# Optimization experiments

Hardware: AMD Instinct MI355X
Metric: run time of the kernel (lower is better)

The kernel has to match this reference:

```python
import jax, jax.numpy as jnp
import numpy as np
import math

CEN_W = 1.0
ANG_W = 1.0


def _radius(ndim):
    # Iterative version of the recursive Radius() from the source.
    if ndim < 1:
        raise ValueError('ndim >= 1 required')
    if ndim == 1:
        return 0.0
    r = 0.5
    for _ in range(3, ndim + 1):
        r = 0.5 / math.sqrt(1.0 - r * r)
    return r


def _costheta(ndim):
    return 2.0 * _radius(ndim - 1) ** 2 - 1.0


def setup_inputs() -> dict:
    key = jax.random.key(0)
    k1, k2, k3 = jax.random.split(key, 3)
    B, C, D = 65536, 1000, 512
    y = jax.random.randint(k1, (B,), 0, C, dtype=jnp.int64 if jax.config.jax_enable_x64 else jnp.int32)
    feat = jax.random.normal(k2, (B, D), dtype=jnp.float32)
    centers = jax.random.normal(k3, (C, D), dtype=jnp.float32)
    return {"y": y, "feat": feat, "centers": centers}


def reference(y, feat, centers):
    C = centers.shape[0]
    B = feat.shape[0]
    ct = jnp.float32(_costheta(C))  # static Python constant from num_classes

    # ---- center loss: gather assigned centers, squared diff sum ----
    centers_pred = centers[y]                      # [B, D] gather
    diff = feat - centers_pred
    loss_cen = 0.5 * jnp.sum(diff * diff) / B

    # ---- angular loss: vectorized Gram matrix over classes ----
    # In torch, centers[j].data and dist are detached -> stop_gradient here.
    centers_sg = jax.lax.stop_gradient(centers)
    dist = jnp.linalg.norm(centers_sg, axis=1)     # [C], detached
    gram = centers @ centers_sg.T                  # [C, C]; grad flows via rows only
    sim = gram / (dist[:, None] * dist[None, :])
    offdiag = 1.0 - jnp.eye(C, dtype=sim.dtype)
    loss_ang = jnp.sum(offdiag * (sim - ct) ** 2) / (0.5 * C * (C - 1))

    return loss_cen * CEN_W + loss_ang * ANG_W
```

## Files before the change

### kernel.cpp

```cpp
#include <hip/hip_runtime.h>
#include <math.h>

typedef __attribute__((ext_vector_type(8))) short bf16x8;
typedef __attribute__((ext_vector_type(4))) float f32x4;

__device__ __forceinline__ float wave_reduce(float v) {
#pragma unroll
    for (int off = 32; off > 0; off >>= 1) v += __shfl_down(v, off, 64);
    return v;
}

__device__ __forceinline__ unsigned short f2bf(float x) {
    unsigned u = __float_as_uint(x);
    u += 0x7FFFu + ((u >> 16) & 1u);
    return (unsigned short)(u >> 16);
}

__global__ __launch_bounds__(128) void prep_kernel(const float4* __restrict__ cent4,
                                                   ushort4* __restrict__ xb,
                                                   float* __restrict__ dist2,
                                                   int C, int d4) {
    const int r = blockIdx.x;
    const int t = threadIdx.x;
    __shared__ float sm[2];
    float s = 0.f;
    for (int c = t; c < d4; c += blockDim.x) {
        float4 f = make_float4(0.f, 0.f, 0.f, 0.f);
        if (r < C) f = cent4[(size_t)r * d4 + c];
        s += f.x * f.x + f.y * f.y + f.z * f.z + f.w * f.w;
        ushort4 h;
        h.x = f2bf(f.x); h.y = f2bf(f.y); h.z = f2bf(f.z); h.w = f2bf(f.w);
        xb[(size_t)r * d4 + c] = h;
    }
    s = wave_reduce(s);
    const int lane = t & 63, w = t >> 6;
    if (lane == 0) sm[w] = s;
    __syncthreads();
    if (t == 0) {
        float tot = sm[0];
        if (blockDim.x > 64) tot += sm[1];
        dist2[r] = (r < C) ? tot : 1.0f;
    }
}

__global__ __launch_bounds__(256) void center_kernel(const int* __restrict__ y,
                                                     const float4* __restrict__ feat4,
                                                     const float4* __restrict__ cent4,
                                                     float* __restrict__ out,
                                                     int n4, int d4, float scale) {
    __shared__ float sm[4];
    const int stride = gridDim.x * 256;
    float s = 0.f;
    int i = blockIdx.x * 256 + threadIdx.x;
    if ((stride % d4) == 0) {
        if (i < n4) {
            int row = i / d4;
            const int col = i - row * d4;
            const int rstep = stride / d4;
            for (; i < n4; i += stride, row += rstep) {
                const int cls = y[row];
                float4 f = feat4[i];
                float4 c = cent4[(size_t)cls * d4 + col];
                float dx = f.x - c.x, dy = f.y - c.y, dz = f.z - c.z, dw = f.w - c.w;
                s += dx * dx + dy * dy + dz * dz + dw * dw;
            }
        }
    } else {
        for (; i < n4; i += stride) {
            int row = i / d4;
            int col = i - row * d4;
            const int cls = y[row];
            float4 f = feat4[i];
            float4 c = cent4[(size_t)cls * d4 + col];
            float dx = f.x - c.x, dy = f.y - c.y, dz = f.z - c.z, dw = f.w - c.w;
            s += dx * dx + dy * dy + dz * dz + dw * dw;
        }
    }
    s = wave_reduce(s);
    const int lane = threadIdx.x & 63, w = threadIdx.x >> 6;
    if (lane == 0) sm[w] = s;
    __syncthreads();
    if (threadIdx.x == 0) {
        float tot = sm[0] + sm[1] + sm[2] + sm[3];
        atomicAdd(out, tot * scale);
    }
}

__global__ __launch_bounds__(256) void ang_kernel(const unsigned short* __restrict__ xb,
                                                  const float* __restrict__ dist2,
                                                  float* __restrict__ out,
                                                  int C, int D, int ntile,
                                                  float ct, float scale) {
    __shared__ float sm[4];
    const int wid = threadIdx.x >> 6;
    const int w = blockIdx.x * 4 + wid;
    float local = 0.f;
    if (w < ntile * ntile) {
        const int ti = w / ntile;
        const int tj = w - ti * ntile;
        const int lane = threadIdx.x & 63;
        const int n = lane & 15;
        const int quad = lane >> 4;
        const int dv = D >> 3;
        const bf16x8* ap = (const bf16x8*)xb + (size_t)(ti * 16 + n) * dv + quad;
        const bf16x8* bp = (const bf16x8*)xb + (size_t)(tj * 16 + n) * dv + quad;
        f32x4 acc = {0.f, 0.f, 0.f, 0.f};
        const int steps = D >> 5;
#pragma unroll 8
        for (int st = 0; st < steps; ++st) {
            bf16x8 a = ap[st * 4];
            bf16x8 b = bp[st * 4];
            acc = __builtin_amdgcn_mfma_f32_16x16x32_bf16(a, b, acc, 0, 0, 0);
        }
        const int gj = tj * 16 + n;
        const float dj = dist2[gj];
#pragma unroll
        for (int rr = 0; rr < 4; ++rr) {
            const int gi = ti * 16 + quad * 4 + rr;
            if (gi < C && gj < C && gi != gj) {
                float sim = acc[rr] * rsqrtf(dist2[gi] * dj);
                float dlt = sim - ct;
                local += dlt * dlt;
            }
        }
    }
    local = wave_reduce(local);
    if ((threadIdx.x & 63) == 0) sm[wid] = local;
    __syncthreads();
    if (threadIdx.x == 0) {
        float tot = sm[0] + sm[1] + sm[2] + sm[3];
        atomicAdd(out, tot * scale);
    }
}

extern "C" void kernel_launch(void* const* d_in, const int* in_sizes, int n_in,
                              void* d_out, int out_size, void* d_ws, size_t ws_size,
                              hipStream_t stream) {
    const int* y = (const int*)d_in[0];
    const float* feat = (const float*)d_in[1];
    const float* centers = (const float*)d_in[2];

    const int B = in_sizes[0];
    const int D = in_sizes[1] / B;
    const int C = in_sizes[2] / D;
    const int d4 = D / 4;
    const int ntile = (C + 15) / 16;
    const int Cpad = ntile * 16;

    const int nd = C - 1;
    double r = 0.0;
    if (nd >= 2) {
        r = 0.5;
        for (int i = 3; i <= nd; ++i) r = 0.5 / sqrt(1.0 - r * r);
    }
    const float ct = (float)(2.0 * r * r - 1.0);

    float* outp = (float*)d_out;
    char* ws = (char*)d_ws;
    unsigned short* xb = (unsigned short*)ws;
    size_t xb_bytes = (size_t)Cpad * D * sizeof(unsigned short);
    float* dist2 = (float*)(ws + ((xb_bytes + 255) & ~(size_t)255));

    hipMemsetAsync(d_out, 0, sizeof(float), stream);

    prep_kernel<<<Cpad, 128, 0, stream>>>((const float4*)centers, (ushort4*)xb, dist2, C, d4);

    const int n4 = B * d4;
    const float cen_scale = (float)(0.5 / (double)B);
    center_kernel<<<2048, 256, 0, stream>>>(y, (const float4*)feat, (const float4*)centers,
                                            outp, n4, d4, cen_scale);

    const int ntile2 = ntile * ntile;
    const int ang_blocks = (ntile2 + 3) / 4;
    const float ang_scale = (float)(1.0 / (0.5 * (double)C * (double)(C - 1)));
    ang_kernel<<<ang_blocks, 256, 0, stream>>>(xb, dist2, outp, C, D, ntile, ct, ang_scale);
}
```

Measured before the change: 244.5 us.

## Fuse center and angular kernels into one launch, fold memset into prep

Combines the center-loss and angular-loss kernels into a single launch, with the block index choosing which branch runs, so the compute-heavy MFMA tiles can overlap the bandwidth-bound gather-and-reduce. The hipMemset of the output is dropped; prep_kernel zeroes it instead, which saves one launch. Feature loads become nontemporal to avoid polluting the cache that the centers gather relies on. The extra branching costs little, and the output stays correctly ordered because prep_kernel still runs before the fused kernel on the same stream.

```diff
diff --git a/kernel.cpp b/kernel.cpp
--- a/kernel.cpp
+++ b/kernel.cpp
@@ -3,6 +3,7 @@
 
 typedef __attribute__((ext_vector_type(8))) short bf16x8;
 typedef __attribute__((ext_vector_type(4))) float f32x4;
+typedef __attribute__((ext_vector_type(4))) float vf4;
 
 __device__ __forceinline__ float wave_reduce(float v) {
 #pragma unroll
@@ -19,9 +20,11 @@
 __global__ __launch_bounds__(128) void prep_kernel(const float4* __restrict__ cent4,
                                                    ushort4* __restrict__ xb,
                                                    float* __restrict__ dist2,
+                                                   float* __restrict__ out,
                                                    int C, int d4) {
     const int r = blockIdx.x;
     const int t = threadIdx.x;
+    if (r == 0 && t == 0) out[0] = 0.f;
     __shared__ float sm[2];
     float s = 0.f;
     for (int c = t; c < d4; c += blockDim.x) {
@@ -43,93 +46,94 @@
     }
 }
 
-__global__ __launch_bounds__(256) void center_kernel(const int* __restrict__ y,
-                                                     const float4* __restrict__ feat4,
-                                                     const float4* __restrict__ cent4,
-                                                     float* __restrict__ out,
-                                                     int n4, int d4, float scale) {
+__global__ __launch_bounds__(256) void fused_kernel(const int* __restrict__ y,
+                                                    const vf4* __restrict__ feat4,
+                                                    const float4* __restrict__ cent4,
+                                                    const unsigned short* __restrict__ xb,
+                                                    const float* __restrict__ dist2,
+                                                    float* __restrict__ out,
+                                                    int n4, int d4, float cen_scale,
+                                                    int C, int D, int ntile,
+                                                    float ct, float ang_scale,
+                                                    int ang_blocks, int center_blocks) {
     __shared__ float sm[4];
-    const int stride = gridDim.x * 256;
-    float s = 0.f;
-    int i = blockIdx.x * 256 + threadIdx.x;
-    if ((stride % d4) == 0) {
-        if (i < n4) {
-            int row = i / d4;
-            const int col = i - row * d4;
-            const int rstep = stride / d4;
-            for (; i < n4; i += stride, row += rstep) {
+    const int lane = threadIdx.x & 63;
+    const int wid = threadIdx.x >> 6;
+
+    if ((int)blockIdx.x < ang_blocks) {
+        const int w = blockIdx.x * 4 + wid;
+        float local = 0.f;
+        if (w < ntile * ntile) {
+            const int ti = w / ntile;
+            const int tj = w - ti * ntile;
+            const int n = lane & 15;
+            const int quad = lane >> 4;
+            const int dv = D >> 3;
+            const bf16x8* ap = (const bf16x8*)xb + (size_t)(ti * 16 + n) * dv + quad;
+            const bf16x8* bp = (const bf16x8*)xb + (size_t)(tj * 16 + n) * dv + quad;
+            f32x4 acc = {0.f, 0.f, 0.f, 0.f};
+            const int steps = D >> 5;
+#pragma unroll 8
+            for (int st = 0; st < steps; ++st) {
+                bf16x8 a = ap[st * 4];
+                bf16x8 b = bp[st * 4];
+                acc = __builtin_amdgcn_mfma_f32_16x16x32_bf16(a, b, acc, 0, 0, 0);
+            }
+            const int gj = tj * 16 + n;
+            const float dj = dist2[gj];
+#pragma unroll
+            for (int rr = 0; rr < 4; ++rr) {
+                const int gi = ti * 16 + quad * 4 + rr;
+                if (gi < C && gj < C && gi != gj) {
+                    float sim = acc[rr] * rsqrtf(dist2[gi] * dj);
+                    float dlt = sim - ct;
+                    local += dlt * dlt;
+                }
+            }
+        }
+        local = wave_reduce(local);
+        if (lane == 0) sm[wid] = local;
+        __syncthreads();
+        if (threadIdx.x == 0) {
+            float tot = sm[0] + sm[1] + sm[2] + sm[3];
+            atomicAdd(out, tot * ang_scale);
+        }
+    } else {
+        const int cb = blockIdx.x - ang_blocks;
+        const int stride = center_blocks * 256;
+        float s = 0.f;
+        int i = cb * 256 + threadIdx.x;
+        if ((stride % d4) == 0) {
+            if (i < n4) {
+                int row = i / d4;
+                const int col = i - row * d4;
+                const int rstep = stride / d4;
+                for (; i < n4; i += stride, row += rstep) {
+                    const int cls = y[row];
+                    vf4 f = __builtin_nontemporal_load(feat4 + i);
+                    float4 c = cent4[(size_t)cls * d4 + col];
+                    float dx = f.x - c.x, dy = f.y - c.y, dz = f.z - c.z, dw = f.w - c.w;
+                    s += dx * dx + dy * dy + dz * dz + dw * dw;
+                }
+            }
+        } else {
+            for (; i < n4; i += stride) {
+                int row = i / d4;
+                int col = i - row * d4;
                 const int cls = y[row];
-                float4 f = feat4[i];
+                vf4 f = __builtin_nontemporal_load(feat4 + i);
                 float4 c = cent4[(size_t)cls * d4 + col];
                 float dx = f.x - c.x, dy = f.y - c.y, dz = f.z - c.z, dw = f.w - c.w;
                 s += dx * dx + dy * dy + dz * dz + dw * dw;
             }
         }
-    } else {
-        for (; i < n4; i += stride) {
-            int row = i / d4;
-            int col = i - row * d4;
-            const int cls = y[row];
-            float4 f = feat4[i];
-            float4 c = cent4[(size_t)cls * d4 + col];
-            float dx = f.x - c.x, dy = f.y - c.y, dz = f.z - c.z, dw = f.w - c.w;
-            s += dx * dx + dy * dy + dz * dz + dw * dw;
+        s = wave_reduce(s);
+        if (lane == 0) sm[wid] = s;
+        __syncthreads();
+        if (threadIdx.x == 0) {
+            float tot = sm[0] + sm[1] + sm[2] + sm[3];
+            atomicAdd(out, tot * cen_scale);
         }
-    }
-    s = wave_reduce(s);
-    const int lane = threadIdx.x & 63, w = threadIdx.x >> 6;
-    if (lane == 0) sm[w] = s;
-    __syncthreads();
-    if (threadIdx.x == 0) {
-        float tot = sm[0] + sm[1] + sm[2] + sm[3];
-        atomicAdd(out, tot * scale);
-    }
-}
-
-__global__ __launch_bounds__(256) void ang_kernel(const unsigned short* __restrict__ xb,
-                                                  const float* __restrict__ dist2,
-                                                  float* __restrict__ out,
-                                                  int C, int D, int ntile,
-                                                  float ct, float scale) {
-    __shared__ float sm[4];
-    const int wid = threadIdx.x >> 6;
-    const int w = blockIdx.x * 4 + wid;
-    float local = 0.f;
-    if (w < ntile * ntile) {
-        const int ti = w / ntile;
-        const int tj = w - ti * ntile;
-        const int lane = threadIdx.x & 63;
-        const int n = lane & 15;
-        const int quad = lane >> 4;
-        const int dv = D >> 3;
-        const bf16x8* ap = (const bf16x8*)xb + (size_t)(ti * 16 + n) * dv + quad;
-        const bf16x8* bp = (const bf16x8*)xb + (size_t)(tj * 16 + n) * dv + quad;
-        f32x4 acc = {0.f, 0.f, 0.f, 0.f};
-        const int steps = D >> 5;
-#pragma unroll 8
-        for (int st = 0; st < steps; ++st) {
-            bf16x8 a = ap[st * 4];
-            bf16x8 b = bp[st * 4];
-            acc = __builtin_amdgcn_mfma_f32_16x16x32_bf16(a, b, acc, 0, 0, 0);
-        }
-        const int gj = tj * 16 + n;
-        const float dj = dist2[gj];
-#pragma unroll
-        for (int rr = 0; rr < 4; ++rr) {
-            const int gi = ti * 16 + quad * 4 + rr;
-            if (gi < C && gj < C && gi != gj) {
-                float sim = acc[rr] * rsqrtf(dist2[gi] * dj);
-                float dlt = sim - ct;
-                local += dlt * dlt;
-            }
-        }
-    }
-    local = wave_reduce(local);
-    if ((threadIdx.x & 63) == 0) sm[wid] = local;
-    __syncthreads();
-    if (threadIdx.x == 0) {
-        float tot = sm[0] + sm[1] + sm[2] + sm[3];
-        atomicAdd(out, tot * scale);
     }
 }
 
@@ -161,17 +165,17 @@
     size_t xb_bytes = (size_t)Cpad * D * sizeof(unsigned short);
     float* dist2 = (float*)(ws + ((xb_bytes + 255) & ~(size_t)255));
 
-    hipMemsetAsync(d_out, 0, sizeof(float), stream);
-
-    prep_kernel<<<Cpad, 128, 0, stream>>>((const float4*)centers, (ushort4*)xb, dist2, C, d4);
+    prep_kernel<<<Cpad, 128, 0, stream>>>((const float4*)centers, (ushort4*)xb, dist2,
+                                          outp, C, d4);
 
     const int n4 = B * d4;
     const float cen_scale = (float)(0.5 / (double)B);
-    center_kernel<<<2048, 256, 0, stream>>>(y, (const float4*)feat, (const float4*)centers,
-                                            outp, n4, d4, cen_scale);
-
+    const float ang_scale = (float)(1.0 / (0.5 * (double)C * (double)(C - 1)));
     const int ntile2 = ntile * ntile;
     const int ang_blocks = (ntile2 + 3) / 4;
-    const float ang_scale = (float)(1.0 / (0.5 * (double)C * (double)(C - 1)));
-    ang_kernel<<<ang_blocks, 256, 0, stream>>>(xb, dist2, outp, C, D, ntile, ct, ang_scale);
+    const int center_blocks = 2048;
+
+    fused_kernel<<<ang_blocks + center_blocks, 256, 0, stream>>>(
+        y, (const vf4*)feat, (const float4*)centers, xb, dist2, outp,
+        n4, d4, cen_scale, C, D, ntile, ct, ang_scale, ang_blocks, center_blocks);
 }
```

Result: faster. 224.5 us (-8.2%).
